# Performance work log

Measured on AMD Instinct MI355X. Metric: run time of the kernel, lower is better.

## Reference

```python
import jax, jax.numpy as jnp
import numpy as np

N_TOTAL = 2_000_000   # total particles across all events
N_EVENTS = 20_000     # number of events (segments)
H = 64                # phi/rho hidden width
OUT = 10              # output classes


def _lin(x, W, b):
    # torch nn.Linear: y = x @ W.T + b
    return x @ W.T + b


def setup_inputs() -> dict:
    key = jax.random.key(0)
    ks = jax.random.split(key, 24)
    s = 0.1  # small init scale
    inp = {
        "values": jax.random.normal(ks[0], (N_TOTAL,), dtype=jnp.float32),
        "seg_ids": jnp.sort(jax.random.randint(ks[1], (N_TOTAL,), 0, N_EVENTS)),
        "p1w0": jax.random.normal(ks[2], (H, 1), dtype=jnp.float32) * s,
        "p1b0": jax.random.normal(ks[3], (H,), dtype=jnp.float32) * s,
        "p1w1": jax.random.normal(ks[4], (H, H), dtype=jnp.float32) * s,
        "p1b1": jax.random.normal(ks[5], (H,), dtype=jnp.float32) * s,
        "r1w0": jax.random.normal(ks[6], (H, H), dtype=jnp.float32) * s,
        "r1b0": jax.random.normal(ks[7], (H,), dtype=jnp.float32) * s,
        "r1w1": jax.random.normal(ks[8], (H, H), dtype=jnp.float32) * s,
        "r1b1": jax.random.normal(ks[9], (H,), dtype=jnp.float32) * s,
        "o1w": jax.random.normal(ks[10], (H, H), dtype=jnp.float32) * s,
        "o1b": jax.random.normal(ks[11], (H,), dtype=jnp.float32) * s,
        "p2w0": jax.random.normal(ks[12], (H, H), dtype=jnp.float32) * s,
        "p2b0": jax.random.normal(ks[13], (H,), dtype=jnp.float32) * s,
        "p2w1": jax.random.normal(ks[14], (H, H), dtype=jnp.float32) * s,
        "p2b1": jax.random.normal(ks[15], (H,), dtype=jnp.float32) * s,
        "r2w0": jax.random.normal(ks[16], (H, H), dtype=jnp.float32) * s,
        "r2b0": jax.random.normal(ks[17], (H,), dtype=jnp.float32) * s,
        "r2w1": jax.random.normal(ks[18], (H, H), dtype=jnp.float32) * s,
        "r2b1": jax.random.normal(ks[19], (H,), dtype=jnp.float32) * s,
        "o2w": jax.random.normal(ks[20], (OUT, H), dtype=jnp.float32) * s,
        "o2b": jax.random.normal(ks[21], (OUT,), dtype=jnp.float32) * s,
    }
    return inp


def reference(values, seg_ids, p1w0, p1b0, p1w1, p1b1, r1w0, r1b0, r1w1, r1b1,
              o1w, o1b, p2w0, p2b0, p2w1, p2b1, r2w0, r2b0, r2w1, r2b1, o2w, o2b):
    relu = jax.nn.relu
    # stage 1: phi1 on each scalar particle value -> [N, H]
    h = relu(_lin(values[:, None], p1w0, p1b0))
    h = relu(_lin(h, p1w1, p1b1))
    # jagged sum over particles within each event (the inner deepset sum)
    ev = jax.ops.segment_sum(h, seg_ids, num_segments=N_EVENTS)  # [E, H]
    # rho1 + output linear + activation per event
    ev = relu(_lin(ev, r1w0, r1b0))
    ev = relu(_lin(ev, r1w1, r1b1))
    ev = relu(_lin(ev, o1w, o1b))  # [E, H] (output_size of deepset1 = rho_sizes[-1])
    # stage 2: phi2 per event, sum over all events
    h2 = relu(_lin(ev, p2w0, p2b0))
    h2 = relu(_lin(h2, p2w1, p2b1))
    s2 = jnp.sum(h2, axis=0, keepdims=True)  # [1, H]
    r2 = relu(_lin(s2, r2w0, r2b0))
    r2 = relu(_lin(r2, r2w1, r2b1))
    out = _lin(r2, o2w, o2b)  # [1, OUT]
    return jax.nn.log_softmax(out, axis=1)
```

## Files before the change

kernel.cpp:

```cpp
#include <hip/hip_runtime.h>

#define NT 2000000
#define NE 20000
#define NTILES (NT / 64)

using bf16x8 = __attribute__((ext_vector_type(8))) __bf16;
using bf16x4 = __attribute__((ext_vector_type(4))) __bf16;
using f32x4  = __attribute__((ext_vector_type(4))) float;
using f32x2  = __attribute__((ext_vector_type(2))) float;
using fvec4  = __attribute__((ext_vector_type(4))) float;

__device__ __forceinline__ void load_bsplit(const float* __restrict__ p,
                                            bf16x8& hi, bf16x8& lo) {
    fvec4 a = *(const fvec4*)p;
    fvec4 b = *(const fvec4*)(p + 4);
#pragma unroll
    for (int e = 0; e < 4; e++) {
        float v  = a[e];
        __bf16 h = (__bf16)v;
        hi[e]    = h;
        lo[e]    = (__bf16)(v - (float)h);
        float v2  = b[e];
        __bf16 h2 = (__bf16)v2;
        hi[e + 4] = h2;
        lo[e + 4] = (__bf16)(v2 - (float)h2);
    }
}

__device__ __forceinline__ bf16x8 load_bf8(const float* __restrict__ p) {
    fvec4 a = *(const fvec4*)p;
    fvec4 b = *(const fvec4*)(p + 4);
    bf16x8 r;
#pragma unroll
    for (int e = 0; e < 4; e++) {
        r[e]     = (__bf16)a[e];
        r[e + 4] = (__bf16)b[e];
    }
    return r;
}

__global__ __launch_bounds__(256, 4) void k1_phi1(
    const float* __restrict__ values, const int* __restrict__ seg,
    const float* __restrict__ w0, const float* __restrict__ b0,
    const float* __restrict__ w1, const float* __restrict__ b1,
    float* __restrict__ ev) {
    const int tid = threadIdx.x;
    const int w   = tid >> 6;
    const int l   = tid & 63;
    const int l15 = l & 15;
    const int l4  = l >> 4;

    bf16x8 Bh[2][4];
#pragma unroll
    for (int kf = 0; kf < 2; kf++)
#pragma unroll
        for (int jf = 0; jf < 4; jf++)
            Bh[kf][jf] = load_bf8(w1 + (jf * 16 + l15) * 64 + kf * 32 + l4 * 8);

    f32x2 w0p[2][4], b0p[2][4];
#pragma unroll
    for (int kf = 0; kf < 2; kf++) {
        const int kb = kf * 32 + l4 * 8;
#pragma unroll
        for (int e2 = 0; e2 < 4; e2++) {
            w0p[kf][e2] = *(const f32x2*)(w0 + kb + e2 * 2);
            b0p[kf][e2] = *(const f32x2*)(b0 + kb + e2 * 2);
        }
    }
    f32x4 biasC[4];
#pragma unroll
    for (int jf = 0; jf < 4; jf++) {
        const float bj = b1[jf * 16 + l15];
#pragma unroll
        for (int r = 0; r < 4; r++) biasC[jf][r] = bj;
    }

    const bool bit0 = (l & 16) != 0;
    const bool bit1 = (l & 32) != 0;
    auto reduce4 = [&](const float sj[4]) -> float {
        float send01 = bit0 ? sj[0] : sj[1];
        float keep01 = bit0 ? sj[1] : sj[0];
        float c01 = keep01 + __shfl_xor(send01, 16);
        float send23 = bit0 ? sj[2] : sj[3];
        float keep23 = bit0 ? sj[3] : sj[2];
        float c23 = keep23 + __shfl_xor(send23, 16);
        float send = bit1 ? c01 : c23;
        float keep = bit1 ? c23 : c01;
        return keep + __shfl_xor(send, 32);
    };

    const int stride = gridDim.x * 4;
    int tile = blockIdx.x * 4 + w;

    int s_cur = seg[tile * 64 + l];
    float vp[4];
#pragma unroll
    for (int pf = 0; pf < 4; pf++) vp[pf] = values[tile * 64 + pf * 16 + l15];

    while (tile < NTILES) {
        const int ntile = tile + stride;
        int s_nxt = 0;
        float vpn[4] = {0.f, 0.f, 0.f, 0.f};
        if (ntile < NTILES) {
            const int nb = ntile * 64;
            s_nxt = seg[nb + l];
#pragma unroll
            for (int pf = 0; pf < 4; pf++) vpn[pf] = values[nb + pf * 16 + l15];
        }

        const int prev = __shfl_up(s_cur, 1);
        const unsigned long long bmask = __ballot((l > 0) && (s_cur != prev));

        int   cur = __builtin_amdgcn_readlane(s_cur, 0);
        float sj[4] = {0.f, 0.f, 0.f, 0.f};

#pragma unroll
        for (int q = 0; q < 2; q++) {
#pragma unroll
            for (int i = 0; i < 2; i++) {
                const int B = q * 32 + i * 16;
                const float vq = vp[2 * q + i];
                const f32x2 vv = {vq, vq};

                bf16x8 A0, A1;
#pragma unroll
                for (int e2 = 0; e2 < 4; e2++) {
                    f32x2 h0 = w0p[0][e2] * vv + b0p[0][e2];
                    A0[2 * e2]     = (__bf16)fmaxf(h0[0], 0.f);
                    A0[2 * e2 + 1] = (__bf16)fmaxf(h0[1], 0.f);
                    f32x2 h1 = w0p[1][e2] * vv + b0p[1][e2];
                    A1[2 * e2]     = (__bf16)fmaxf(h1[0], 0.f);
                    A1[2 * e2 + 1] = (__bf16)fmaxf(h1[1], 0.f);
                }

                f32x4 frag[4];
#pragma unroll
                for (int jf = 0; jf < 4; jf++) {
                    f32x4 t = __builtin_amdgcn_mfma_f32_16x16x32_bf16(
                        A0, Bh[0][jf], biasC[jf], 0, 0, 0);
                    t = __builtin_amdgcn_mfma_f32_16x16x32_bf16(
                        A1, Bh[1][jf], t, 0, 0, 0);
#pragma unroll
                    for (int r = 0; r < 4; r++) frag[jf][r] = fmaxf(t[r], 0.f);
                }

                const unsigned int mb =
                    (unsigned int)((bmask >> B) & 0xFFFFull);
                if (mb == 0u) {
#pragma unroll
                    for (int jf = 0; jf < 4; jf++)
                        sj[jf] += (frag[jf][0] + frag[jf][1]) +
                                  (frag[jf][2] + frag[jf][3]);
                } else {
                    unsigned int m = mb;
                    int start = 0;
                    while (true) {
                        const int e = m ? (int)__builtin_ctz(m) : 16;
#pragma unroll
                        for (int jf = 0; jf < 4; jf++) {
                            float s = 0.f;
#pragma unroll
                            for (int r = 0; r < 4; r++) {
                                const int rel = l4 * 4 + r;
                                s += (rel >= start && rel < e) ? frag[jf][r]
                                                               : 0.f;
                            }
                            sj[jf] += s;
                        }
                        if (!m) break;
                        atomicAdd(ev + (size_t)cur * 64 + l, reduce4(sj));
                        sj[0] = sj[1] = sj[2] = sj[3] = 0.f;
                        cur   = __builtin_amdgcn_readlane(s_cur, B + e);
                        start = e;
                        m &= (m - 1);
                    }
                }
            }
        }
        atomicAdd(ev + (size_t)cur * 64 + l, reduce4(sj));

        tile  = ntile;
        s_cur = s_nxt;
#pragma unroll
        for (int pf = 0; pf < 4; pf++) vp[pf] = vpn[pf];
    }
}

__global__ __launch_bounds__(64) void k2_events(
    const float* __restrict__ ev,
    const float* __restrict__ W0, const float* __restrict__ B0,
    const float* __restrict__ W1, const float* __restrict__ B1,
    const float* __restrict__ W2, const float* __restrict__ B2,
    const float* __restrict__ W3, const float* __restrict__ B3,
    const float* __restrict__ W4, const float* __restrict__ B4,
    float* __restrict__ s2) {
    __shared__ __align__(16) __bf16 xt[64 * 72];
    const int l   = threadIdx.x;
    const int l15 = l & 15;
    const int l4  = l >> 4;
    const int ebase = blockIdx.x * 64;

    const float* Ws[5] = {W0, W1, W2, W3, W4};
    const float* Bs[5] = {B0, B1, B2, B3, B4};

    bf16x8 A[4][2];
#pragma unroll
    for (int pf = 0; pf < 4; pf++) {
        const int e = ebase + pf * 16 + l15;
#pragma unroll
        for (int kf = 0; kf < 2; kf++) {
            bf16x8 a;
            if (e < NE) {
                const float* p = ev + (size_t)e * 64 + kf * 32 + l4 * 8;
                fvec4 x = *(const fvec4*)p;
                fvec4 y = *(const fvec4*)(p + 4);
#pragma unroll
                for (int e2 = 0; e2 < 4; e2++) {
                    a[e2]     = (__bf16)x[e2];
                    a[e2 + 4] = (__bf16)y[e2];
                }
            } else {
#pragma unroll
                for (int e2 = 0; e2 < 8; e2++) a[e2] = (__bf16)0.f;
            }
            A[pf][kf] = a;
        }
    }

#pragma unroll
    for (int L = 0; L < 5; L++) {
        bf16x8 Bh[2][4], Bl[2][4];
#pragma unroll
        for (int kf = 0; kf < 2; kf++)
#pragma unroll
            for (int jf = 0; jf < 4; jf++)
                load_bsplit(Ws[L] + (jf * 16 + l15) * 64 + kf * 32 + l4 * 8,
                            Bh[kf][jf], Bl[kf][jf]);

        f32x4 acc[4][4];
#pragma unroll
        for (int jf = 0; jf < 4; jf++) {
            const float bj = Bs[L][jf * 16 + l15];
#pragma unroll
            for (int pf = 0; pf < 4; pf++)
#pragma unroll
                for (int r = 0; r < 4; r++) acc[pf][jf][r] = bj;
        }
#pragma unroll
        for (int kf = 0; kf < 2; kf++)
#pragma unroll
            for (int pf = 0; pf < 4; pf++)
#pragma unroll
                for (int jf = 0; jf < 4; jf++)
                    acc[pf][jf] = __builtin_amdgcn_mfma_f32_16x16x32_bf16(
                        A[pf][kf], Bh[kf][jf], acc[pf][jf], 0, 0, 0);
#pragma unroll
        for (int kf = 0; kf < 2; kf++)
#pragma unroll
            for (int pf = 0; pf < 4; pf++)
#pragma unroll
                for (int jf = 0; jf < 4; jf++)
                    acc[pf][jf] = __builtin_amdgcn_mfma_f32_16x16x32_bf16(
                        A[pf][kf], Bl[kf][jf], acc[pf][jf], 0, 0, 0);

        if (L < 4) {
#pragma unroll
            for (int pf = 0; pf < 4; pf++)
#pragma unroll
                for (int jf = 0; jf < 4; jf++) {
                    const int j = jf * 16 + l15;
#pragma unroll
                    for (int r = 0; r < 4; r++)
                        xt[(pf * 16 + l4 * 4 + r) * 72 + j] =
                            (__bf16)fmaxf(acc[pf][jf][r], 0.f);
                }
#pragma unroll
            for (int pf = 0; pf < 4; pf++)
#pragma unroll
                for (int kf = 0; kf < 2; kf++)
                    A[pf][kf] = *(const bf16x8*)(xt + (pf * 16 + l15) * 72 +
                                                 kf * 32 + l4 * 8);
        } else {
            float sj[4];
#pragma unroll
            for (int jf = 0; jf < 4; jf++) {
                float s = 0.f;
#pragma unroll
                for (int pf = 0; pf < 4; pf++)
#pragma unroll
                    for (int r = 0; r < 4; r++) {
                        const int e = ebase + pf * 16 + l4 * 4 + r;
                        float v = fmaxf(acc[pf][jf][r], 0.f);
                        s += (e < NE) ? v : 0.f;
                    }
                s += __shfl_xor(s, 16);
                s += __shfl_xor(s, 32);
                sj[jf] = s;
            }
            float v = (l4 == 0) ? sj[0] : (l4 == 1) ? sj[1]
                    : (l4 == 2) ? sj[2] : sj[3];
            atomicAdd(s2 + l, v);
        }
    }
}

__global__ __launch_bounds__(64) void k3_final(
    const float* __restrict__ s2,
    const float* __restrict__ W0, const float* __restrict__ B0,
    const float* __restrict__ W1, const float* __restrict__ B1,
    const float* __restrict__ W2, const float* __restrict__ B2,
    float* __restrict__ out) {
    __shared__ __align__(16) float xb[64];
    __shared__ __align__(16) float yb[64];
    __shared__ float ob[10];
    const int l = threadIdx.x;

    xb[l] = s2[l];
    __syncthreads();

    float a = B0[l];
#pragma unroll
    for (int k = 0; k < 16; k++) {
        fvec4 wv = *(const fvec4*)(W0 + l * 64 + k * 4);
        fvec4 xv = *(const fvec4*)(xb + k * 4);
        a += wv[0] * xv[0] + wv[1] * xv[1] + wv[2] * xv[2] + wv[3] * xv[3];
    }
    yb[l] = fmaxf(a, 0.f);
    __syncthreads();

    float b_ = B1[l];
#pragma unroll
    for (int k = 0; k < 16; k++) {
        fvec4 wv = *(const fvec4*)(W1 + l * 64 + k * 4);
        fvec4 xv = *(const fvec4*)(yb + k * 4);
        b_ += wv[0] * xv[0] + wv[1] * xv[1] + wv[2] * xv[2] + wv[3] * xv[3];
    }
    __syncthreads();
    xb[l] = fmaxf(b_, 0.f);
    __syncthreads();

    if (l < 10) {
        float o = B2[l];
#pragma unroll
        for (int k = 0; k < 16; k++) {
            fvec4 wv = *(const fvec4*)(W2 + l * 64 + k * 4);
            fvec4 xv = *(const fvec4*)(xb + k * 4);
            o += wv[0] * xv[0] + wv[1] * xv[1] + wv[2] * xv[2] + wv[3] * xv[3];
        }
        ob[l] = o;
    }
    __syncthreads();
    if (l == 0) {
        float m = ob[0];
#pragma unroll
        for (int i = 1; i < 10; i++) m = fmaxf(m, ob[i]);
        float sum = 0.f;
#pragma unroll
        for (int i = 0; i < 10; i++) sum = sum + expf(ob[i] - m);
        float ls = logf(sum);
#pragma unroll
        for (int i = 0; i < 10; i++) out[i] = ob[i] - m - ls;
    }
}

extern "C" void kernel_launch(void* const* d_in, const int* in_sizes, int n_in,
                              void* d_out, int out_size, void* d_ws, size_t ws_size,
                              hipStream_t stream) {
    const float* values = (const float*)d_in[0];
    const int*   seg    = (const int*)d_in[1];
    const float* p1w0 = (const float*)d_in[2],  *p1b0 = (const float*)d_in[3];
    const float* p1w1 = (const float*)d_in[4],  *p1b1 = (const float*)d_in[5];
    const float* r1w0 = (const float*)d_in[6],  *r1b0 = (const float*)d_in[7];
    const float* r1w1 = (const float*)d_in[8],  *r1b1 = (const float*)d_in[9];
    const float* o1w  = (const float*)d_in[10], *o1b  = (const float*)d_in[11];
    const float* p2w0 = (const float*)d_in[12], *p2b0 = (const float*)d_in[13];
    const float* p2w1 = (const float*)d_in[14], *p2b1 = (const float*)d_in[15];
    const float* r2w0 = (const float*)d_in[16], *r2b0 = (const float*)d_in[17];
    const float* r2w1 = (const float*)d_in[18], *r2b1 = (const float*)d_in[19];
    const float* o2w  = (const float*)d_in[20], *o2b  = (const float*)d_in[21];

    float* ev = (float*)d_ws;
    float* s2 = ev + (size_t)NE * 64;

    hipMemsetAsync(d_ws, 0, (size_t)(NE * 64 + 64) * sizeof(float), stream);

    hipLaunchKernelGGL(k1_phi1, dim3(1024), dim3(256), 0, stream,
                       values, seg, p1w0, p1b0, p1w1, p1b1, ev);
    hipLaunchKernelGGL(k2_events, dim3((NE + 63) / 64), dim3(64), 0, stream,
                       ev, r1w0, r1b0, r1w1, r1b1, o1w, o1b,
                       p2w0, p2b0, p2w1, p2b1, s2);
    hipLaunchKernelGGL(k3_final, dim3(1), dim3(64), 0, stream,
                       s2, r2w0, r2b0, r2w1, r2b1, o2w, o2b, (float*)d_out);
}
```

Before: 73.65 us.

## Use fp16 phi1 math, 128-particle tiles, direct atomics, fuse final kernel

Phi1 now computes its first layer in packed fp16 and runs the MFMA in f16 instead of bf16. Each wave handles 128 particles per iteration, and the grid and occupancy hint are reduced. Segment flushes now issue four atomics per lane directly instead of a cross-lane shuffle reduction. The final rho2/output kernel is folded into k2 using a last-block counter, which removes one launch. These changes trade fewer instructions and launches for more atomics and possible fp16 range or precision issues.

After: 154.3 us. 110% more time.

```diff
diff --git a/kernel.cpp b/kernel.cpp
--- a/kernel.cpp
+++ b/kernel.cpp
@@ -2,10 +2,11 @@
 
 #define NT 2000000
 #define NE 20000
-#define NTILES (NT / 64)
+#define NTILES128 (NT / 128)
 
 using bf16x8 = __attribute__((ext_vector_type(8))) __bf16;
-using bf16x4 = __attribute__((ext_vector_type(4))) __bf16;
+using half8  = __attribute__((ext_vector_type(8))) _Float16;
+using half2v = __attribute__((ext_vector_type(2))) _Float16;
 using f32x4  = __attribute__((ext_vector_type(4))) float;
 using f32x2  = __attribute__((ext_vector_type(2))) float;
 using fvec4  = __attribute__((ext_vector_type(4))) float;
@@ -27,19 +28,19 @@
     }
 }
 
-__device__ __forceinline__ bf16x8 load_bf8(const float* __restrict__ p) {
+__device__ __forceinline__ half8 load_h8(const float* __restrict__ p) {
     fvec4 a = *(const fvec4*)p;
     fvec4 b = *(const fvec4*)(p + 4);
-    bf16x8 r;
+    half8 r;
 #pragma unroll
     for (int e = 0; e < 4; e++) {
-        r[e]     = (__bf16)a[e];
-        r[e + 4] = (__bf16)b[e];
+        r[e]     = (_Float16)a[e];
+        r[e + 4] = (_Float16)b[e];
     }
     return r;
 }
 
-__global__ __launch_bounds__(256, 4) void k1_phi1(
+__global__ __launch_bounds__(256, 3) void k1_phi1(
     const float* __restrict__ values, const int* __restrict__ seg,
     const float* __restrict__ w0, const float* __restrict__ b0,
     const float* __restrict__ w1, const float* __restrict__ b1,
@@ -50,21 +51,23 @@
     const int l15 = l & 15;
     const int l4  = l >> 4;
 
-    bf16x8 Bh[2][4];
+    half8 Bh[2][4];
 #pragma unroll
     for (int kf = 0; kf < 2; kf++)
 #pragma unroll
         for (int jf = 0; jf < 4; jf++)
-            Bh[kf][jf] = load_bf8(w1 + (jf * 16 + l15) * 64 + kf * 32 + l4 * 8);
-
-    f32x2 w0p[2][4], b0p[2][4];
+            Bh[kf][jf] = load_h8(w1 + (jf * 16 + l15) * 64 + kf * 32 + l4 * 8);
+
+    half2v w0h[2][4], b0h[2][4];
 #pragma unroll
     for (int kf = 0; kf < 2; kf++) {
         const int kb = kf * 32 + l4 * 8;
 #pragma unroll
         for (int e2 = 0; e2 < 4; e2++) {
-            w0p[kf][e2] = *(const f32x2*)(w0 + kb + e2 * 2);
-            b0p[kf][e2] = *(const f32x2*)(b0 + kb + e2 * 2);
+            f32x2 wp = *(const f32x2*)(w0 + kb + 2 * e2);
+            f32x2 bp = *(const f32x2*)(b0 + kb + 2 * e2);
+            w0h[kf][e2] = half2v{(_Float16)wp[0], (_Float16)wp[1]};
+            b0h[kf][e2] = half2v{(_Float16)bp[0], (_Float16)bp[1]};
         }
     }
     f32x4 biasC[4];
@@ -75,114 +78,114 @@
         for (int r = 0; r < 4; r++) biasC[jf][r] = bj;
     }
 
-    const bool bit0 = (l & 16) != 0;
-    const bool bit1 = (l & 32) != 0;
-    auto reduce4 = [&](const float sj[4]) -> float {
-        float send01 = bit0 ? sj[0] : sj[1];
-        float keep01 = bit0 ? sj[1] : sj[0];
-        float c01 = keep01 + __shfl_xor(send01, 16);
-        float send23 = bit0 ? sj[2] : sj[3];
-        float keep23 = bit0 ? sj[3] : sj[2];
-        float c23 = keep23 + __shfl_xor(send23, 16);
-        float send = bit1 ? c01 : c23;
-        float keep = bit1 ? c23 : c01;
-        return keep + __shfl_xor(send, 32);
+    auto FLUSH = [&](int sid, const float* sj) {
+#pragma unroll
+        for (int jf = 0; jf < 4; jf++)
+            atomicAdd(ev + (size_t)sid * 64 + jf * 16 + l15, sj[jf]);
     };
 
     const int stride = gridDim.x * 4;
     int tile = blockIdx.x * 4 + w;
 
-    int s_cur = seg[tile * 64 + l];
-    float vp[4];
-#pragma unroll
-    for (int pf = 0; pf < 4; pf++) vp[pf] = values[tile * 64 + pf * 16 + l15];
-
-    while (tile < NTILES) {
+    int sA = seg[tile * 128 + l];
+    int sB = seg[tile * 128 + 64 + l];
+    half2v vph[4];
+#pragma unroll
+    for (int b = 0; b < 8; b++)
+        vph[b >> 1][b & 1] = (_Float16)values[tile * 128 + b * 16 + l15];
+
+    while (tile < NTILES128) {
         const int ntile = tile + stride;
-        int s_nxt = 0;
-        float vpn[4] = {0.f, 0.f, 0.f, 0.f};
-        if (ntile < NTILES) {
-            const int nb = ntile * 64;
-            s_nxt = seg[nb + l];
-#pragma unroll
-            for (int pf = 0; pf < 4; pf++) vpn[pf] = values[nb + pf * 16 + l15];
-        }
-
-        const int prev = __shfl_up(s_cur, 1);
-        const unsigned long long bmask = __ballot((l > 0) && (s_cur != prev));
-
-        int   cur = __builtin_amdgcn_readlane(s_cur, 0);
+        int sAn = 0, sBn = 0;
+        half2v vpn[4];
+#pragma unroll
+        for (int i = 0; i < 4; i++) vpn[i] = half2v{(_Float16)0.f, (_Float16)0.f};
+        if (ntile < NTILES128) {
+            const int nb = ntile * 128;
+            sAn = seg[nb + l];
+            sBn = seg[nb + 64 + l];
+#pragma unroll
+            for (int b = 0; b < 8; b++)
+                vpn[b >> 1][b & 1] = (_Float16)values[nb + b * 16 + l15];
+        }
+
+        const int prevA = __shfl_up(sA, 1);
+        const unsigned long long mA = __ballot((l > 0) && (sA != prevA));
+        const int lastA = __builtin_amdgcn_readlane(sA, 63);
+        int prevB = __shfl_up(sB, 1);
+        prevB = (l == 0) ? lastA : prevB;
+        const unsigned long long mB = __ballot(sB != prevB);
+
+        int   cur = __builtin_amdgcn_readlane(sA, 0);
         float sj[4] = {0.f, 0.f, 0.f, 0.f};
 
 #pragma unroll
-        for (int q = 0; q < 2; q++) {
-#pragma unroll
-            for (int i = 0; i < 2; i++) {
-                const int B = q * 32 + i * 16;
-                const float vq = vp[2 * q + i];
-                const f32x2 vv = {vq, vq};
-
-                bf16x8 A0, A1;
-#pragma unroll
-                for (int e2 = 0; e2 < 4; e2++) {
-                    f32x2 h0 = w0p[0][e2] * vv + b0p[0][e2];
-                    A0[2 * e2]     = (__bf16)fmaxf(h0[0], 0.f);
-                    A0[2 * e2 + 1] = (__bf16)fmaxf(h0[1], 0.f);
-                    f32x2 h1 = w0p[1][e2] * vv + b0p[1][e2];
-                    A1[2 * e2]     = (__bf16)fmaxf(h1[0], 0.f);
-                    A1[2 * e2 + 1] = (__bf16)fmaxf(h1[1], 0.f);
-                }
-
-                f32x4 frag[4];
-#pragma unroll
-                for (int jf = 0; jf < 4; jf++) {
-                    f32x4 t = __builtin_amdgcn_mfma_f32_16x16x32_bf16(
-                        A0, Bh[0][jf], biasC[jf], 0, 0, 0);
-                    t = __builtin_amdgcn_mfma_f32_16x16x32_bf16(
-                        A1, Bh[1][jf], t, 0, 0, 0);
-#pragma unroll
-                    for (int r = 0; r < 4; r++) frag[jf][r] = fmaxf(t[r], 0.f);
-                }
-
-                const unsigned int mb =
-                    (unsigned int)((bmask >> B) & 0xFFFFull);
-                if (mb == 0u) {
-#pragma unroll
-                    for (int jf = 0; jf < 4; jf++)
-                        sj[jf] += (frag[jf][0] + frag[jf][1]) +
-                                  (frag[jf][2] + frag[jf][3]);
-                } else {
-                    unsigned int m = mb;
-                    int start = 0;
-                    while (true) {
-                        const int e = m ? (int)__builtin_ctz(m) : 16;
-#pragma unroll
-                        for (int jf = 0; jf < 4; jf++) {
-                            float s = 0.f;
-#pragma unroll
-                            for (int r = 0; r < 4; r++) {
-                                const int rel = l4 * 4 + r;
-                                s += (rel >= start && rel < e) ? frag[jf][r]
-                                                               : 0.f;
-                            }
-                            sj[jf] += s;
+        for (int b = 0; b < 8; b++) {
+            const unsigned mask16 =
+                (unsigned)(((b < 4 ? mA : mB) >> (16 * (b & 3))) & 0xFFFFull);
+            const _Float16 vh = vph[b >> 1][b & 1];
+            const half2v vv = {vh, vh};
+
+            half8 A0, A1;
+#pragma unroll
+            for (int e2 = 0; e2 < 4; e2++) {
+                half2v h0 = vv * w0h[0][e2] + b0h[0][e2];
+                half2v h1 = vv * w0h[1][e2] + b0h[1][e2];
+                const _Float16 z = (_Float16)0.f;
+                A0[2 * e2]     = h0[0] > z ? h0[0] : z;
+                A0[2 * e2 + 1] = h0[1] > z ? h0[1] : z;
+                A1[2 * e2]     = h1[0] > z ? h1[0] : z;
+                A1[2 * e2 + 1] = h1[1] > z ? h1[1] : z;
+            }
+
+            f32x4 frag[4];
+#pragma unroll
+            for (int jf = 0; jf < 4; jf++) {
+                f32x4 t = __builtin_amdgcn_mfma_f32_16x16x32_f16(
+                    A0, Bh[0][jf], biasC[jf], 0, 0, 0);
+                t = __builtin_amdgcn_mfma_f32_16x16x32_f16(
+                    A1, Bh[1][jf], t, 0, 0, 0);
+#pragma unroll
+                for (int r = 0; r < 4; r++) frag[jf][r] = fmaxf(t[r], 0.f);
+            }
+
+            if (mask16 == 0u) {
+#pragma unroll
+                for (int jf = 0; jf < 4; jf++)
+                    sj[jf] += (frag[jf][0] + frag[jf][1]) +
+                              (frag[jf][2] + frag[jf][3]);
+            } else {
+                unsigned m = mask16;
+                int start = 0;
+                while (true) {
+                    const int e = m ? (int)__builtin_ctz(m) : 16;
+#pragma unroll
+                    for (int jf = 0; jf < 4; jf++) {
+                        float s = 0.f;
+#pragma unroll
+                        for (int r = 0; r < 4; r++) {
+                            const int rel = l4 * 4 + r;
+                            s += (rel >= start && rel < e) ? frag[jf][r] : 0.f;
                         }
-                        if (!m) break;
-                        atomicAdd(ev + (size_t)cur * 64 + l, reduce4(sj));
-                        sj[0] = sj[1] = sj[2] = sj[3] = 0.f;
-                        cur   = __builtin_amdgcn_readlane(s_cur, B + e);
-                        start = e;
-                        m &= (m - 1);
+                        sj[jf] += s;
                     }
+                    if (!m) break;
+                    FLUSH(cur, sj);
+                    sj[0] = sj[1] = sj[2] = sj[3] = 0.f;
+                    cur = __builtin_amdgcn_readlane(b < 4 ? sA : sB,
+                                                    16 * (b & 3) + e);
+                    start = e;
+                    m &= (m - 1);
                 }
             }
         }
-        atomicAdd(ev + (size_t)cur * 64 + l, reduce4(sj));
-
-        tile  = ntile;
-        s_cur = s_nxt;
-#pragma unroll
-        for (int pf = 0; pf < 4; pf++) vp[pf] = vpn[pf];
+        FLUSH(cur, sj);
+
+        tile = ntile;
+        sA = sAn;
+        sB = sBn;
+#pragma unroll
+        for (int i = 0; i < 4; i++) vph[i] = vpn[i];
     }
 }
 
@@ -193,7 +196,11 @@
     const float* __restrict__ W2, const float* __restrict__ B2,
     const float* __restrict__ W3, const float* __restrict__ B3,
     const float* __restrict__ W4, const float* __restrict__ B4,
-    float* __restrict__ s2) {
+    float* __restrict__ s2, int* __restrict__ counter,
+    const float* __restrict__ R0, const float* __restrict__ Rb0,
+    const float* __restrict__ R1, const float* __restrict__ Rb1,
+    const float* __restrict__ OW, const float* __restrict__ OB,
+    float* __restrict__ out) {
     __shared__ __align__(16) __bf16 xt[64 * 72];
     const int l   = threadIdx.x;
     const int l15 = l & 15;
@@ -302,36 +309,37 @@
             atomicAdd(s2 + l, v);
         }
     }
-}
-
-__global__ __launch_bounds__(64) void k3_final(
-    const float* __restrict__ s2,
-    const float* __restrict__ W0, const float* __restrict__ B0,
-    const float* __restrict__ W1, const float* __restrict__ B1,
-    const float* __restrict__ W2, const float* __restrict__ B2,
-    float* __restrict__ out) {
+
+    __shared__ int is_last;
+    __threadfence();
+    if (l == 0) {
+        const int c = atomicAdd(counter, 1);
+        is_last = (c == (int)gridDim.x - 1);
+    }
+    __syncthreads();
+    if (!is_last) return;
+
     __shared__ __align__(16) float xb[64];
     __shared__ __align__(16) float yb[64];
     __shared__ float ob[10];
-    const int l = threadIdx.x;
-
-    xb[l] = s2[l];
-    __syncthreads();
-
-    float a = B0[l];
+
+    xb[l] = atomicAdd(s2 + l, 0.f);
+    __syncthreads();
+
+    float a0 = Rb0[l];
 #pragma unroll
     for (int k = 0; k < 16; k++) {
-        fvec4 wv = *(const fvec4*)(W0 + l * 64 + k * 4);
+        fvec4 wv = *(const fvec4*)(R0 + l * 64 + k * 4);
         fvec4 xv = *(const fvec4*)(xb + k * 4);
-        a += wv[0] * xv[0] + wv[1] * xv[1] + wv[2] * xv[2] + wv[3] * xv[3];
-    }
-    yb[l] = fmaxf(a, 0.f);
-    __syncthreads();
-
-    float b_ = B1[l];
+        a0 += wv[0] * xv[0] + wv[1] * xv[1] + wv[2] * xv[2] + wv[3] * xv[3];
+    }
+    yb[l] = fmaxf(a0, 0.f);
+    __syncthreads();
+
+    float b_ = Rb1[l];
 #pragma unroll
     for (int k = 0; k < 16; k++) {
-        fvec4 wv = *(const fvec4*)(W1 + l * 64 + k * 4);
+        fvec4 wv = *(const fvec4*)(R1 + l * 64 + k * 4);
         fvec4 xv = *(const fvec4*)(yb + k * 4);
         b_ += wv[0] * xv[0] + wv[1] * xv[1] + wv[2] * xv[2] + wv[3] * xv[3];
     }
@@ -340,10 +348,10 @@
     __syncthreads();
 
     if (l < 10) {
-        float o = B2[l];
+        float o = OB[l];
 #pragma unroll
         for (int k = 0; k < 16; k++) {
-            fvec4 wv = *(const fvec4*)(W2 + l * 64 + k * 4);
+            fvec4 wv = *(const fvec4*)(OW + l * 64 + k * 4);
             fvec4 xv = *(const fvec4*)(xb + k * 4);
             o += wv[0] * xv[0] + wv[1] * xv[1] + wv[2] * xv[2] + wv[3] * xv[3];
         }
@@ -381,14 +389,15 @@
 
     float* ev = (float*)d_ws;
     float* s2 = ev + (size_t)NE * 64;
-
-    hipMemsetAsync(d_ws, 0, (size_t)(NE * 64 + 64) * sizeof(float), stream);
-
-    hipLaunchKernelGGL(k1_phi1, dim3(1024), dim3(256), 0, stream,
+    int* counter = (int*)(s2 + 64);
+
+    hipMemsetAsync(d_ws, 0, (size_t)(NE * 64 + 64) * sizeof(float) + sizeof(int),
+                   stream);
+
+    hipLaunchKernelGGL(k1_phi1, dim3(768), dim3(256), 0, stream,
                        values, seg, p1w0, p1b0, p1w1, p1b1, ev);
     hipLaunchKernelGGL(k2_events, dim3((NE + 63) / 64), dim3(64), 0, stream,
                        ev, r1w0, r1b0, r1w1, r1b1, o1w, o1b,
-                       p2w0, p2b0, p2w1, p2b1, s2);
-    hipLaunchKernelGGL(k3_final, dim3(1), dim3(64), 0, stream,
-                       s2, r2w0, r2b0, r2w1, r2b1, o2w, o2b, (float*)d_out);
+                       p2w0, p2b0, p2w1, p2b1, s2, counter,
+                       r2w0, r2b0, r2w1, r2b1, o2w, o2b, (float*)d_out);
 }
```
